# Kernel tuning notes

Hardware: AMD Instinct MI355X
Metric: run time of the kernel (lower is better)

## Reference

```python
import jax, jax.numpy as jnp
import numpy as np

B = 1024           # number of drug pairs (graphs per side)
ATOMS = 64         # atoms per molecule
N = B * ATOMS      # total atoms per side
H = 512            # hidden_size * number_of_molecules
FFN_H = 2048
OUT = 86           # num_tasks


def setup_inputs() -> dict:
    key = jax.random.key(0)
    ks = jax.random.split(key, 12)
    inv = 1.0 / np.sqrt(H)
    inv2 = 1.0 / np.sqrt(2 * H)
    invf = 1.0 / np.sqrt(FFN_H)
    return {
        "left_output": jax.random.normal(ks[0], (B, H), jnp.float32),
        "right_output": jax.random.normal(ks[1], (B, H), jnp.float32),
        "left_atom": jax.random.normal(ks[2], (N, H), jnp.float32),
        "right_atom": jax.random.normal(ks[3], (N, H), jnp.float32),
        "left_batch": jnp.arange(N, dtype=jnp.int32) // ATOMS,
        "right_batch": jnp.arange(N, dtype=jnp.int32) // ATOMS,
        "noise": jax.random.uniform(ks[4], (B, H), jnp.float32),
        "w_i_w": jax.random.normal(ks[5], (H, H), jnp.float32) * inv,
        "w_i_b": jnp.zeros((H,), jnp.float32),
        "prj_i_w": jax.random.normal(ks[6], (H, H), jnp.float32) * inv,
        "prj_i_b": jnp.zeros((H,), jnp.float32),
        "ffn1_w": jax.random.normal(ks[7], (2 * H, FFN_H), jnp.float32) * inv2,
        "ffn1_b": jnp.zeros((FFN_H,), jnp.float32),
        "ffn2_w": jax.random.normal(ks[8], (FFN_H, OUT), jnp.float32) * invf,
        "ffn2_b": jnp.zeros((OUT,), jnp.float32),
    }


def _seg_softmax(s, seg, num_segments):
    m = jax.ops.segment_max(s, seg, num_segments=num_segments)
    e = jnp.exp(s - m[seg])
    z = jax.ops.segment_sum(e, seg, num_segments=num_segments)
    return e / z[seg]


def reference(left_output, right_output, left_atom, right_atom,
              left_batch, right_batch, noise,
              w_i_w, w_i_b, prj_i_w, prj_i_b,
              ffn1_w, ffn1_b, ffn2_w, ffn2_b):
    # repeat_interleave(left_output, degree(right_batch)) == gather by segment id
    left_align = left_output[right_batch]    # [N_r, H]
    right_align = right_output[left_batch]   # [N_l, H]

    # cross-molecule coattention scores (elementwise product + reduce)
    left_scores = jnp.sum((left_atom @ w_i_w + w_i_b) * (right_align @ prj_i_w + prj_i_b), axis=-1)
    left_scores = _seg_softmax(left_scores, left_batch, B)
    right_scores = jnp.sum((right_atom @ w_i_w + w_i_b) * (left_align @ prj_i_w + prj_i_b), axis=-1)
    right_scores = _seg_softmax(right_scores, right_batch, B)

    # attention-weighted global add pool
    h_output = jax.ops.segment_sum(left_atom * right_align * left_scores[:, None], left_batch, num_segments=B)
    t_output = jax.ops.segment_sum(right_atom * left_align * right_scores[:, None], right_batch, num_segments=B)

    # sign-directed noise perturbation (same noise for both sides, as in original)
    nrm = jnp.maximum(jnp.linalg.norm(noise, axis=-1, keepdims=True), 1e-12)
    noise_n = noise / nrm
    h_pert = h_output + jnp.sign(h_output) * noise_n * 0.1
    t_pert = t_output + jnp.sign(t_output) * noise_n * 0.1

    pair = jnp.concatenate([h_pert, t_pert], axis=-1)  # [B, 2H]
    hid = jax.nn.relu(pair @ ffn1_w + ffn1_b)
    output = hid @ ffn2_w + ffn2_b  # training mode: raw logits, no sigmoid
    return (output, h_output, h_pert, left_scores, right_scores, left_output, right_output)
```

## Files before the change

kernel.cpp:

```cpp
#include <hip/hip_runtime.h>
#include <hip/hip_bf16.h>
#include <float.h>

#define B_ 1024
#define H_ 512
#define N_ (B_ * 64)
#define FFN_ 2048
#define OUT_ 86

typedef __bf16 bf16_t;
typedef __attribute__((ext_vector_type(8))) __bf16 bf16x8;
typedef __attribute__((ext_vector_type(4))) float f32x4;

__device__ __forceinline__ float wred_sum(float v) {
#pragma unroll
  for (int m = 32; m; m >>= 1) v += __shfl_xor(v, m);
  return v;
}
__device__ __forceinline__ float wred_max(float v) {
#pragma unroll
  for (int m = 32; m; m >>= 1) v = fmaxf(v, __shfl_xor(v, m));
  return v;
}

__device__ __forceinline__ void gload_lds16(const void* g, void* l) {
  __builtin_amdgcn_global_load_lds((const __attribute__((address_space(1))) unsigned int*)g,
                                   (__attribute__((address_space(3))) unsigned int*)l, 16, 0, 0);
}

template <bool BT, bool BIAS>
__global__ __launch_bounds__(256) void gemm64(const float* __restrict__ A1, const float* __restrict__ A2,
                                              int M1, const float* __restrict__ Bm,
                                              const float* __restrict__ bias, float* __restrict__ C,
                                              int N, int K) {
  __shared__ float As[16][68];
  __shared__ float Bs[16][68];
  const int bm = blockIdx.x * 64, bn = blockIdx.y * 64;
  const float* __restrict__ A = (bm < M1) ? (A1 + (size_t)bm * K) : (A2 + (size_t)(bm - M1) * K);
  const int t = threadIdx.x;
  const int tx = t & 15, ty = t >> 4;
  float acc[4][4] = {};
  for (int k0 = 0; k0 < K; k0 += 16) {
#pragma unroll
    for (int i = 0; i < 4; i++) {
      int m = (t >> 4) + i * 16;
      As[t & 15][m] = A[(size_t)m * K + k0 + (t & 15)];
    }
    if (BT) {
#pragma unroll
      for (int i = 0; i < 4; i++) {
        int n = (t >> 4) + i * 16;
        Bs[t & 15][n] = Bm[(size_t)(bn + n) * K + k0 + (t & 15)];
      }
    } else {
#pragma unroll
      for (int i = 0; i < 4; i++) {
        int kk = (t >> 6) + i * 4;
        Bs[kk][t & 63] = Bm[(size_t)(k0 + kk) * N + bn + (t & 63)];
      }
    }
    __syncthreads();
#pragma unroll
    for (int kk = 0; kk < 16; kk++) {
      float4 av = *(const float4*)&As[kk][ty * 4];
      float4 bv = *(const float4*)&Bs[kk][tx * 4];
      float a_[4] = {av.x, av.y, av.z, av.w};
      float b_[4] = {bv.x, bv.y, bv.z, bv.w};
#pragma unroll
      for (int i = 0; i < 4; i++)
#pragma unroll
        for (int j = 0; j < 4; j++) acc[i][j] += a_[i] * b_[j];
    }
    __syncthreads();
  }
#pragma unroll
  for (int i = 0; i < 4; i++) {
    int m = bm + ty * 4 + i;
    float tmp[4];
#pragma unroll
    for (int j = 0; j < 4; j++) {
      float x = acc[i][j];
      if (BIAS) x += bias[bn + tx * 4 + j];
      tmp[j] = x;
    }
    float4 v;
    v.x = tmp[0]; v.y = tmp[1]; v.z = tmp[2]; v.w = tmp[3];
    *(float4*)&C[(size_t)m * N + bn + tx * 4] = v;
  }
}

__global__ __launch_bounds__(256, 2) void k_atoms9(const float* __restrict__ atomL, const float* __restrict__ atomR,
                                                   const float* __restrict__ uLR,
                                                   float* __restrict__ scoresL, float* __restrict__ scoresR,
                                                   float* __restrict__ pL, float* __restrict__ pR) {
  const int pair = blockIdx.x;
  const int side = pair >> 10, b = pair & 1023;
  const int t = threadIdx.x, wave = t >> 6, lane = t & 63;

  __shared__ float s_all[64];
  __shared__ float s_nrm[64];
  __shared__ float pp[4][512];

  const float* __restrict__ atom = side ? atomR : atomL;
  const float* __restrict__ u = uLR + (size_t)pair * H_;
  f32x4 u0 = *(const f32x4*)&u[lane * 4];
  f32x4 u1 = *(const f32x4*)&u[256 + lane * 4];

  const float* __restrict__ base = atom + ((size_t)b * 64 + wave * 16) * H_ + lane * 4;

  f32x4 A0[16], A1[16];
#pragma unroll
  for (int i = 0; i < 16; i++) {
    const float* r0 = base + (size_t)i * H_;
    asm volatile("global_load_dwordx4 %0, %1, off" : "=&v"(A0[i]) : "v"(r0) : "memory");
    asm volatile("global_load_dwordx4 %0, %1, off" : "=&v"(A1[i]) : "v"(r0 + 256) : "memory");
  }
  asm volatile("s_waitcnt vmcnt(0)" ::: "memory");
  __builtin_amdgcn_sched_barrier(0);

  float d[16];
#pragma unroll
  for (int i = 0; i < 16; i++)
    d[i] = A0[i].x * u0.x + A0[i].y * u0.y + A0[i].z * u0.z + A0[i].w * u0.w +
           A1[i].x * u1.x + A1[i].y * u1.y + A1[i].z * u1.z + A1[i].w * u1.w;
#pragma unroll
  for (int i = 0; i < 16; i++) d[i] = wred_sum(d[i]);
  if (lane < 16) {
    float myv = 0.f;
#pragma unroll
    for (int i = 0; i < 16; i++) myv = (lane == i) ? d[i] : myv;
    s_all[wave * 16 + lane] = myv;
  }
  __syncthreads();

  {
    float sv = s_all[lane];
    float M = wred_max(sv);
    float e = __expf(sv - M);
    float Z = wred_sum(e);
    float w_n = e / Z;
    if (wave == 0) {
      s_nrm[lane] = w_n;
      (side ? scoresR : scoresL)[(size_t)b * 64 + lane] = w_n;
    }
  }
  __syncthreads();

  f32x4 q0 = {0.f, 0.f, 0.f, 0.f}, q1 = {0.f, 0.f, 0.f, 0.f};
#pragma unroll
  for (int i = 0; i < 16; i++) {
    const float w = s_nrm[wave * 16 + i];
    q0.x += w * A0[i].x; q0.y += w * A0[i].y; q0.z += w * A0[i].z; q0.w += w * A0[i].w;
    q1.x += w * A1[i].x; q1.y += w * A1[i].y; q1.z += w * A1[i].z; q1.w += w * A1[i].w;
  }
  *(f32x4*)&pp[wave][lane * 4] = q0;
  *(f32x4*)&pp[wave][256 + lane * 4] = q1;
  __syncthreads();

  float v0 = pp[0][t] + pp[1][t] + pp[2][t] + pp[3][t];
  float v1 = pp[0][t + 256] + pp[1][t + 256] + pp[2][t + 256] + pp[3][t + 256];
  float* p = (side ? pR : pL) + (size_t)b * H_;
  p[t] = v0;
  p[t + 256] = v1;
}

__global__ __launch_bounds__(512) void k_pert(const float* __restrict__ lo, const float* __restrict__ ro,
                                              const float* __restrict__ noise,
                                              const float* __restrict__ pL, const float* __restrict__ pR,
                                              float* __restrict__ h_out, float* __restrict__ h_pert,
                                              bf16_t* __restrict__ pairbf) {
  const int b = blockIdx.x, t = threadIdx.x;
  float nv = noise[(size_t)b * H_ + t];
  float sq = nv * nv;
  sq = wred_sum(sq);
  __shared__ float red[8];
  if ((t & 63) == 0) red[t >> 6] = sq;
  __syncthreads();
  float tot = 0.f;
#pragma unroll
  for (int i = 0; i < 8; i++) tot += red[i];
  float nrm = fmaxf(sqrtf(tot), 1e-12f);
  float nn = nv / nrm * 0.1f;
  float h = ro[(size_t)b * H_ + t] * pL[(size_t)b * H_ + t];
  float tt = lo[(size_t)b * H_ + t] * pR[(size_t)b * H_ + t];
  float sh = (h > 0.f) ? 1.f : ((h < 0.f) ? -1.f : 0.f);
  float st = (tt > 0.f) ? 1.f : ((tt < 0.f) ? -1.f : 0.f);
  float hp = h + sh * nn;
  float tp = tt + st * nn;
  h_out[(size_t)b * H_ + t] = h;
  h_pert[(size_t)b * H_ + t] = hp;
  pairbf[(size_t)b * 1024 + t] = (bf16_t)hp;
  pairbf[(size_t)b * 1024 + 512 + t] = (bf16_t)tp;
}

__global__ __launch_bounds__(256) void k_w1t(const float* __restrict__ W1, bf16_t* __restrict__ W1t) {
  __shared__ float tile[32][33];
  const int bx = blockIdx.x;
  const int by = blockIdx.y;
  const int tx = threadIdx.x & 31, ty = threadIdx.x >> 5;
#pragma unroll
  for (int i = ty; i < 32; i += 8)
    tile[i][tx] = W1[(size_t)(by * 32 + i) * FFN_ + bx * 32 + tx];
  __syncthreads();
#pragma unroll
  for (int i = ty; i < 32; i += 8)
    W1t[(size_t)(bx * 32 + i) * 1024 + by * 32 + tx] = (bf16_t)tile[tx][i];
}

__global__ __launch_bounds__(256) void k_ffn1(const bf16_t* __restrict__ Abf, const bf16_t* __restrict__ Bt,
                                              const float* __restrict__ bias, float* __restrict__ C) {
  __shared__ bf16_t As[64 * 64];
  __shared__ bf16_t Bs[64 * 64];
  const int bm = blockIdx.x * 64, bn = blockIdx.y * 64;
  const int t = threadIdx.x;
  const int lane = t & 63, wave = t >> 6;
  const int wm = wave & 1, wn = wave >> 1;
  const int l15 = lane & 15, l4 = lane >> 4;
  f32x4 acc[2][2] = {{{0.f, 0.f, 0.f, 0.f}, {0.f, 0.f, 0.f, 0.f}},
                     {{0.f, 0.f, 0.f, 0.f}, {0.f, 0.f, 0.f, 0.f}}};

  for (int k0 = 0; k0 < 1024; k0 += 64) {
#pragma unroll
    for (int r = 0; r < 2; r++) {
      const int off = (r * 256 + t) * 16;
      const int row = off >> 7;
      const int g = (off >> 4) & 7;
      const int scb = ((g ^ (row & 7)) << 4);
      gload_lds16((const char*)Abf + (size_t)(bm + row) * 2048 + k0 * 2 + scb, (char*)As + off);
      gload_lds16((const char*)Bt + (size_t)(bn + row) * 2048 + k0 * 2 + scb, (char*)Bs + off);
    }
    __syncthreads();
#pragma unroll
    for (int ks = 0; ks < 2; ks++) {
      const int ar0 = wm * 32 + l15, ar1 = ar0 + 16;
      const int br0 = wn * 32 + l15, br1 = br0 + 16;
      const int gA = ks * 4 + l4;
      bf16x8 a0 = *(const bf16x8*)((const char*)As + ar0 * 128 + ((gA ^ (ar0 & 7)) << 4));
      bf16x8 a1 = *(const bf16x8*)((const char*)As + ar1 * 128 + ((gA ^ (ar1 & 7)) << 4));
      bf16x8 b0 = *(const bf16x8*)((const char*)Bs + br0 * 128 + ((gA ^ (br0 & 7)) << 4));
      bf16x8 b1 = *(const bf16x8*)((const char*)Bs + br1 * 128 + ((gA ^ (br1 & 7)) << 4));
      acc[0][0] = __builtin_amdgcn_mfma_f32_16x16x32_bf16(a0, b0, acc[0][0], 0, 0, 0);
      acc[0][1] = __builtin_amdgcn_mfma_f32_16x16x32_bf16(a0, b1, acc[0][1], 0, 0, 0);
      acc[1][0] = __builtin_amdgcn_mfma_f32_16x16x32_bf16(a1, b0, acc[1][0], 0, 0, 0);
      acc[1][1] = __builtin_amdgcn_mfma_f32_16x16x32_bf16(a1, b1, acc[1][1], 0, 0, 0);
    }
    __syncthreads();
  }
#pragma unroll
  for (int mi = 0; mi < 2; mi++)
#pragma unroll
    for (int nj = 0; nj < 2; nj++)
#pragma unroll
      for (int r = 0; r < 4; r++) {
        const int m = bm + wm * 32 + mi * 16 + l4 * 4 + r;
        const int n = bn + wn * 32 + nj * 16 + l15;
        float v = acc[mi][nj][r] + bias[n];
        C[(size_t)m * FFN_ + n] = fmaxf(v, 0.f);
      }
}

__global__ void k_w2t(const float* __restrict__ W2, float* __restrict__ W2t) {
  int idx = blockIdx.x * 256 + threadIdx.x;
  if (idx < OUT_ * FFN_) {
    int n = idx / FFN_, k = idx % FFN_;
    W2t[idx] = W2[(size_t)k * OUT_ + n];
  }
}

__global__ __launch_bounds__(256) void k_ffn2(const float* __restrict__ hid, const float* __restrict__ W2t,
                                              const float* __restrict__ b2, float* __restrict__ out) {
  const int b0 = blockIdx.x * 2;
  const int t = threadIdx.x, wave = t >> 6, lane = t & 63;
  float4 h0[8], h1[8];
  const float* r0 = hid + (size_t)b0 * FFN_;
#pragma unroll
  for (int j = 0; j < 8; j++) {
    h0[j] = *(const float4*)&r0[lane * 4 + j * 256];
    h1[j] = *(const float4*)&r0[FFN_ + lane * 4 + j * 256];
  }
  for (int n = wave; n < OUT_; n += 4) {
    const float* wrow = W2t + (size_t)n * FFN_;
    float s0 = 0.f, s1 = 0.f;
#pragma unroll
    for (int j = 0; j < 8; j++) {
      float4 w4 = *(const float4*)&wrow[lane * 4 + j * 256];
      s0 += w4.x * h0[j].x + w4.y * h0[j].y + w4.z * h0[j].z + w4.w * h0[j].w;
      s1 += w4.x * h1[j].x + w4.y * h1[j].y + w4.z * h1[j].z + w4.w * h1[j].w;
    }
    s0 = wred_sum(s0);
    s1 = wred_sum(s1);
    if (lane == 0) {
      out[(size_t)b0 * OUT_ + n] = s0 + b2[n];
      out[(size_t)(b0 + 1) * OUT_ + n] = s1 + b2[n];
    }
  }
}

extern "C" void kernel_launch(void* const* d_in, const int* in_sizes, int n_in,
                              void* d_out, int out_size, void* d_ws, size_t ws_size,
                              hipStream_t stream) {
  const float* lo = (const float*)d_in[0];
  const float* ro = (const float*)d_in[1];
  const float* la = (const float*)d_in[2];
  const float* ra = (const float*)d_in[3];
  const float* noise = (const float*)d_in[6];
  const float* w_i_w = (const float*)d_in[7];
  const float* prj_w = (const float*)d_in[9];
  const float* prj_b = (const float*)d_in[10];
  const float* W1 = (const float*)d_in[11];
  const float* b1 = (const float*)d_in[12];
  const float* W2 = (const float*)d_in[13];
  const float* b2 = (const float*)d_in[14];

  float* out = (float*)d_out;
  float* o_logits = out;
  float* o_hout  = out + 88064;
  float* o_hpert = o_hout + 524288;
  float* o_ls    = o_hpert + 524288;
  float* o_rs    = o_ls + 65536;
  float* o_lo    = o_rs + 65536;
  float* o_ro    = o_lo + 524288;

  float* ws = (float*)d_ws;
  float* T    = ws; ws += 2048 * 512;
  float* uLR  = ws; ws += 2048 * 512;
  float* pL   = ws; ws += B_ * H_;
  float* pR   = ws; ws += B_ * H_;
  float* hid  = ws; ws += B_ * FFN_;
  float* W2t  = ws; ws += OUT_ * FFN_;
  bf16_t* pairbf = (bf16_t*)ws; ws += B_ * 1024 / 2;
  bf16_t* W1t    = (bf16_t*)ws; ws += FFN_ * 1024 / 2;

  gemm64<false, true><<<dim3(32, 8), 256, 0, stream>>>(ro, lo, 1024, prj_w, prj_b, T, 512, 512);
  gemm64<true, false><<<dim3(32, 8), 256, 0, stream>>>(T, T, 1 << 30, w_i_w, nullptr, uLR, 512, 512);
  k_w1t<<<dim3(64, 32), 256, 0, stream>>>(W1, W1t);
  k_atoms9<<<2048, 256, 0, stream>>>(la, ra, uLR, o_ls, o_rs, pL, pR);
  k_pert<<<1024, 512, 0, stream>>>(lo, ro, noise, pL, pR, o_hout, o_hpert, pairbf);
  k_ffn1<<<dim3(16, 32), 256, 0, stream>>>(pairbf, W1t, b1, hid);
  k_w2t<<<688, 256, 0, stream>>>(W2, W2t);
  k_ffn2<<<512, 256, 0, stream>>>(hid, W2t, b2, o_logits);
  hipMemcpyAsync(o_lo, lo, (size_t)B_ * H_ * 4, hipMemcpyDeviceToDevice, stream);
  hipMemcpyAsync(o_ro, ro, (size_t)B_ * H_ * 4, hipMemcpyDeviceToDevice, stream);
}
```

Measured before the change: 163.3 us.

## Stream atom rows through a 4-deep register ring and reload for pooling

The atom kernel no longer keeps all 16 rows per wave resident in registers. It now pipelines loads through a 4-slot ring with staged vmcnt waits, and raises the launch bound from 2 to 4 blocks per CU. Because the rows are gone by the pooling pass, they are read a second time from global memory, which should mostly hit cache. The aim is higher occupancy and overlap of loads with dot products, at the cost of doubling the atom reads (about 268 MB of input).

```diff
diff --git a/kernel.cpp b/kernel.cpp
--- a/kernel.cpp
+++ b/kernel.cpp
@@ -89,10 +89,10 @@
   }
 }
 
-__global__ __launch_bounds__(256, 2) void k_atoms9(const float* __restrict__ atomL, const float* __restrict__ atomR,
-                                                   const float* __restrict__ uLR,
-                                                   float* __restrict__ scoresL, float* __restrict__ scoresR,
-                                                   float* __restrict__ pL, float* __restrict__ pR) {
+__global__ __launch_bounds__(256, 4) void k_atoms10(const float* __restrict__ atomL, const float* __restrict__ atomR,
+                                                    const float* __restrict__ uLR,
+                                                    float* __restrict__ scoresL, float* __restrict__ scoresR,
+                                                    float* __restrict__ pL, float* __restrict__ pR) {
   const int pair = blockIdx.x;
   const int side = pair >> 10, b = pair & 1023;
   const int t = threadIdx.x, wave = t >> 6, lane = t & 63;
@@ -108,21 +108,33 @@
 
   const float* __restrict__ base = atom + ((size_t)b * 64 + wave * 16) * H_ + lane * 4;
 
-  f32x4 A0[16], A1[16];
+  f32x4 R0[4], R1[4];
+#pragma unroll
+  for (int r = 0; r < 4; r++) {
+    const float* rp = base + (size_t)r * H_;
+    asm volatile("global_load_dwordx4 %0, %1, off" : "=&v"(R0[r]) : "v"(rp) : "memory");
+    asm volatile("global_load_dwordx4 %0, %1, off" : "=&v"(R1[r]) : "v"(rp + 256) : "memory");
+  }
+
+  float d[16];
 #pragma unroll
   for (int i = 0; i < 16; i++) {
-    const float* r0 = base + (size_t)i * H_;
-    asm volatile("global_load_dwordx4 %0, %1, off" : "=&v"(A0[i]) : "v"(r0) : "memory");
-    asm volatile("global_load_dwordx4 %0, %1, off" : "=&v"(A1[i]) : "v"(r0 + 256) : "memory");
-  }
-  asm volatile("s_waitcnt vmcnt(0)" ::: "memory");
-  __builtin_amdgcn_sched_barrier(0);
-
-  float d[16];
-#pragma unroll
-  for (int i = 0; i < 16; i++)
-    d[i] = A0[i].x * u0.x + A0[i].y * u0.y + A0[i].z * u0.z + A0[i].w * u0.w +
-           A1[i].x * u1.x + A1[i].y * u1.y + A1[i].z * u1.z + A1[i].w * u1.w;
+    if (i <= 12)      asm volatile("s_waitcnt vmcnt(6)" ::: "memory");
+    else if (i == 13) asm volatile("s_waitcnt vmcnt(4)" ::: "memory");
+    else if (i == 14) asm volatile("s_waitcnt vmcnt(2)" ::: "memory");
+    else              asm volatile("s_waitcnt vmcnt(0)" ::: "memory");
+    __builtin_amdgcn_sched_barrier(0);
+    const int s = i & 3;
+    d[i] = R0[s].x * u0.x + R0[s].y * u0.y + R0[s].z * u0.z + R0[s].w * u0.w +
+           R1[s].x * u1.x + R1[s].y * u1.y + R1[s].z * u1.z + R1[s].w * u1.w;
+    __builtin_amdgcn_sched_barrier(0);
+    if (i + 4 < 16) {
+      const float* rp = base + (size_t)(i + 4) * H_;
+      asm volatile("global_load_dwordx4 %0, %1, off" : "=&v"(R0[s]) : "v"(rp) : "memory");
+      asm volatile("global_load_dwordx4 %0, %1, off" : "=&v"(R1[s]) : "v"(rp + 256) : "memory");
+    }
+  }
+
 #pragma unroll
   for (int i = 0; i < 16; i++) d[i] = wred_sum(d[i]);
   if (lane < 16) {
@@ -132,7 +144,6 @@
     s_all[wave * 16 + lane] = myv;
   }
   __syncthreads();
-
   {
     float sv = s_all[lane];
     float M = wred_max(sv);
@@ -150,8 +161,10 @@
 #pragma unroll
   for (int i = 0; i < 16; i++) {
     const float w = s_nrm[wave * 16 + i];
-    q0.x += w * A0[i].x; q0.y += w * A0[i].y; q0.z += w * A0[i].z; q0.w += w * A0[i].w;
-    q1.x += w * A1[i].x; q1.y += w * A1[i].y; q1.z += w * A1[i].z; q1.w += w * A1[i].w;
+    f32x4 x0 = *(const f32x4*)(base + (size_t)i * H_);
+    f32x4 x1 = *(const f32x4*)(base + (size_t)i * H_ + 256);
+    q0.x += w * x0.x; q0.y += w * x0.y; q0.z += w * x0.z; q0.w += w * x0.w;
+    q1.x += w * x1.x; q1.y += w * x1.y; q1.z += w * x1.z; q1.w += w * x1.w;
   }
   *(f32x4*)&pp[wave][lane * 4] = q0;
   *(f32x4*)&pp[wave][256 + lane * 4] = q1;
@@ -334,7 +347,7 @@
   gemm64<false, true><<<dim3(32, 8), 256, 0, stream>>>(ro, lo, 1024, prj_w, prj_b, T, 512, 512);
   gemm64<true, false><<<dim3(32, 8), 256, 0, stream>>>(T, T, 1 << 30, w_i_w, nullptr, uLR, 512, 512);
   k_w1t<<<dim3(64, 32), 256, 0, stream>>>(W1, W1t);
-  k_atoms9<<<2048, 256, 0, stream>>>(la, ra, uLR, o_ls, o_rs, pL, pR);
+  k_atoms10<<<2048, 256, 0, stream>>>(la, ra, uLR, o_ls, o_rs, pL, pR);
   k_pert<<<1024, 512, 0, stream>>>(lo, ro, noise, pL, pR, o_hout, o_hpert, pairbf);
   k_ffn1<<<dim3(16, 32), 256, 0, stream>>>(pairbf, W1t, b1, hid);
   k_w2t<<<688, 256, 0, stream>>>(W2, W2t);
```

Measured after the change: 206.6 us. +26.5%, slower.
